# Performance work log

Hardware: AMD Instinct MI355X
Metric: run time of the kernel (lower is better)

Reference implementation:

```python
import jax, jax.numpy as jnp
import numpy as np
from jax import lax

B, T, I, H = 256, 512, 64, 512

def _uniform(key, shape, scale):
    return jax.random.uniform(key, shape, jnp.float32, -scale, scale)

def setup_inputs() -> dict:
    key = jax.random.key(0)
    ks = jax.random.split(key, 11)
    s = 1.0 / np.sqrt(H)
    return {
        "x": jax.random.normal(ks[0], (B, T, I), jnp.float32),
        "W_ih0": _uniform(ks[1], (4 * H, I), s),
        "W_hh0": _uniform(ks[2], (4 * H, H), s),
        "b_ih0": _uniform(ks[3], (4 * H,), s),
        "b_hh0": _uniform(ks[4], (4 * H,), s),
        "W_ih1": _uniform(ks[5], (4 * H, H), s),
        "W_hh1": _uniform(ks[6], (4 * H, H), s),
        "b_ih1": _uniform(ks[7], (4 * H,), s),
        "b_hh1": _uniform(ks[8], (4 * H,), s),
        "W_fc": _uniform(ks[9], (1, H), s),
        "b_fc": _uniform(ks[10], (1,), s),
    }

def _lstm_layer(x, W_ih, W_hh, b_ih, b_hh):
    # x: [B, T, in]; PyTorch gate order: i, f, g, o
    b, t, _ = x.shape
    h = W_hh.shape[1]
    # precompute input contribution for all timesteps: [B, T, 4H]
    xg = jnp.einsum('bti,gi->btg', x, W_ih) + b_ih + b_hh

    def step(carry, xg_t):
        h_prev, c_prev = carry
        gates = xg_t + h_prev @ W_hh.T  # [B, 4H]
        i_g, f_g, g_g, o_g = jnp.split(gates, 4, axis=-1)
        i_g = jax.nn.sigmoid(i_g)
        f_g = jax.nn.sigmoid(f_g)
        g_g = jnp.tanh(g_g)
        o_g = jax.nn.sigmoid(o_g)
        c = f_g * c_prev + i_g * g_g
        h_new = o_g * jnp.tanh(c)
        return (h_new, c), h_new

    init = (jnp.zeros((b, h), x.dtype), jnp.zeros((b, h), x.dtype))
    _, hs = lax.scan(step, init, xg.transpose(1, 0, 2))  # [T, B, H]
    return hs.transpose(1, 0, 2)  # [B, T, H]

def reference(x, W_ih0, W_hh0, b_ih0, b_hh0, W_ih1, W_hh1, b_ih1, b_hh1, W_fc, b_fc):
    out = _lstm_layer(x, W_ih0, W_hh0, b_ih0, b_hh0)
    # dropout p=0.0 between layers / before fc -> identity (eval semantics)
    out = _lstm_layer(out, W_ih1, W_hh1, b_ih1, b_hh1)
    hidden = out[:, -1, :]  # [B, H]
    return hidden @ W_fc.T + b_fc  # [B, 1]
```

## Files before the change

### kernel.cpp

```cpp
#include <hip/hip_runtime.h>

typedef __bf16 bf16x8 __attribute__((ext_vector_type(8)));
typedef float f32x4 __attribute__((ext_vector_type(4)));
typedef unsigned short u16;
typedef u16 ushort8 __attribute__((ext_vector_type(8)));

#define BB 256
#define TT 512
#define II 64
#define HH 512
#define SLOT 131072

#define OFF_H1RING 0x100000
#define OFF_H1FIN  0x180000
#define OFF_BAR    0x200000
#define OFF_XFRAG  0x210000
#define WS_NEED    (0x210000 + (size_t)(1 << 24))

__device__ __forceinline__ u16 f2bf(float f) {
  unsigned u = __builtin_bit_cast(unsigned, f);
  u = (u + 0x7FFFu + ((u >> 16) & 1u)) >> 16;
  return (u16)u;
}
__device__ __forceinline__ float sigmf(float v) {
  return 1.0f / (1.0f + __expf(-v));
}
__device__ __forceinline__ float tanh_s(float v) {
  float a = __builtin_fabsf(v);
  float e = __expf(-2.0f * a);
  float t = (1.0f - e) / (1.0f + e);
  return __builtin_copysignf(t, v);
}
__device__ __forceinline__ f32x4 mfma16(bf16x8 a, bf16x8 b, f32x4 c) {
  return __builtin_amdgcn_mfma_f32_16x16x32_bf16(a, b, c, 0, 0, 0);
}
__device__ __forceinline__ size_t fragoff(int R, int kk, int lane) {
  return ((size_t)(R * 16 + kk) * 64 + lane) * 8;
}
__device__ __forceinline__ bf16x8 ld_h8(const u16* p) {
  union { unsigned long long q[2]; ushort8 v; } u;
  u.q[0] = __hip_atomic_load((unsigned long long*)p, __ATOMIC_RELAXED,
                             __HIP_MEMORY_SCOPE_AGENT);
  u.q[1] = __hip_atomic_load((unsigned long long*)(p + 4), __ATOMIC_RELAXED,
                             __HIP_MEMORY_SCOPE_AGENT);
  return __builtin_bit_cast(bf16x8, u.v);
}
__device__ __forceinline__ bf16x8 ld_lds8(const u16* p) {
  return __builtin_bit_cast(bf16x8, *(const ushort8*)p);
}

__global__ void init_bar_k(unsigned* bar) {
  for (int i = threadIdx.x; i < 4096; i += blockDim.x) bar[i] = 0u;
}

__global__ void xpose_k(const float* __restrict__ x, u16* __restrict__ xfrag) {
  const size_t idx = (size_t)blockIdx.x * 256 + threadIdx.x;
  const int lane = idx & 63;
  const int kk = (idx >> 6) & 1;
  const int R = (idx >> 7) & 15;
  const int t = (int)(idx >> 11);
  const int row = R * 16 + (lane & 15);
  const int col = kk * 32 + (lane >> 4) * 8;
  const float* src = x + ((size_t)row * TT + t) * II + col;
  ushort8 v;
#pragma unroll
  for (int j = 0; j < 8; ++j) v[j] = f2bf(src[j]);
  *(ushort8*)(xfrag + idx * 8) = v;
}

__global__ __launch_bounds__(256, 1) void lstm_persist(
    const float* __restrict__ x, const u16* __restrict__ xfrag,
    const float* __restrict__ Wih0, const float* __restrict__ Whh0,
    const float* __restrict__ bih0, const float* __restrict__ bhh0,
    const float* __restrict__ Wih1, const float* __restrict__ Whh1,
    const float* __restrict__ bih1, const float* __restrict__ bhh1,
    u16* __restrict__ h0ring, u16* __restrict__ h1ring,
    float* __restrict__ h1fin, unsigned* __restrict__ barA,
    unsigned* __restrict__ barB) {
  __shared__ u16 w0s[32 * 600];
  __shared__ u16 w1s[32 * 1048];

  const int tid = threadIdx.x;
  const int lane = tid & 63;
  const int wid = tid >> 6;
  const int bid = blockIdx.x;
  const int ut = bid & 63, bt = bid >> 6;
  const int u0 = ut * 8;
  const int cc = lane & 15, grp = lane >> 4;

  unsigned* slotsA = barA + (size_t)bt * 256;
  unsigned* slotsB = barB + (size_t)bt * 256;

  {
    const int srow = tid >> 3, sub = tid & 7;
    const int g = (srow >> 3) * 512 + u0 + (srow & 7);
    const float* wih = Wih0 + (size_t)g * 64;
    const float* whh = Whh0 + (size_t)g * 512;
    const int e0 = sub * 72;
    for (int e = e0; e < e0 + 72; ++e) {
      float v = (e < 64) ? wih[e] : whh[e - 64];
      w0s[srow * 600 + e] = f2bf(v);
    }
  }
  {
    const int srow = tid >> 3, sub = tid & 7;
    const int g = (srow >> 3) * 512 + u0 + (srow & 7);
    const float* wih = Wih1 + (size_t)g * 512;
    const float* whh = Whh1 + (size_t)g * 512;
    const int e0 = sub * 128;
    for (int e = e0; e < e0 + 128; ++e) {
      float v = (e < 512) ? wih[e] : whh[e - 512];
      w1s[srow * 1048 + e] = f2bf(v);
    }
  }

  float bias0[2], bias1[2];
#pragma unroll
  for (int nf = 0; nf < 2; ++nf) {
    const int srow = nf * 16 + cc;
    const int g = (srow >> 3) * 512 + u0 + (srow & 7);
    bias0[nf] = bih0[g] + bhh0[g];
    bias1[nf] = bih1[g] + bhh1[g];
  }

  const int row0 = bt * 64 + wid * 16;
  const int Rw = bt * 4 + wid;
  const int arow = row0 + cc;
  const float* xbase = x + (size_t)arow * (TT * II) + grp * 8;
  const bool usexf = (xfrag != nullptr);
  float c0[4] = {0.f, 0.f, 0.f, 0.f};
  float c1[4] = {0.f, 0.f, 0.f, 0.f};

  ushort8 xpre[2];
  float xr[16];
  if (usexf) {
#pragma unroll
    for (int kk = 0; kk < 2; ++kk)
      xpre[kk] = *(const ushort8*)(xfrag + (size_t)Rw * 1024 +
                                   (size_t)kk * 512 + lane * 8);
  } else {
#pragma unroll
    for (int j = 0; j < 16; ++j) xr[j] = xbase[(j >> 3) * 32 + (j & 7)];
  }

  const int kkw = ut >> 2, lpb = (ut & 3) * 16;
  const int lb = grp * 8;

  __syncthreads();

#pragma unroll 1
  for (int s = 0; s <= 513; ++s) {
    const bool doL0 = (s < 512);
    bf16x8 hf[16];

    if (doL0) {
      f32x4 a00 = {bias0[0], bias0[0], bias0[0], bias0[0]};
      f32x4 a01 = {bias0[1], bias0[1], bias0[1], bias0[1]};
      bf16x8 xf[2];
      if (usexf) {
#pragma unroll
        for (int kk = 0; kk < 2; ++kk)
          xf[kk] = __builtin_bit_cast(bf16x8, xpre[kk]);
        const size_t sp = (size_t)((s + 1) & 511);
#pragma unroll
        for (int kk = 0; kk < 2; ++kk)
          xpre[kk] = *(const ushort8*)(xfrag + (sp * 16 + Rw) * 1024 +
                                       (size_t)kk * 512 + lane * 8);
      } else {
#pragma unroll
        for (int kk = 0; kk < 2; ++kk) {
          ushort8 t;
#pragma unroll
          for (int j = 0; j < 8; ++j) t[j] = f2bf(xr[kk * 8 + j]);
          xf[kk] = __builtin_bit_cast(bf16x8, t);
        }
        const size_t sp = (size_t)((s + 1) & 511);
#pragma unroll
        for (int j = 0; j < 16; ++j)
          xr[j] = xbase[sp * II + (j >> 3) * 32 + (j & 7)];
      }
      if (s >= 1) {
        const u16* p = h0ring + (size_t)((s - 1) & 3) * SLOT +
                       fragoff(Rw, 0, lane);
#pragma unroll
        for (int kk = 0; kk < 16; ++kk) hf[kk] = ld_h8(p + (size_t)kk * 512);
      }
#pragma unroll
      for (int kk = 0; kk < 2; ++kk) {
        bf16x8 bA = ld_lds8(&w0s[cc * 600 + kk * 32 + lb]);
        bf16x8 bB = ld_lds8(&w0s[(16 + cc) * 600 + kk * 32 + lb]);
        a00 = mfma16(xf[kk], bA, a00);
        a01 = mfma16(xf[kk], bB, a01);
      }
      if (s >= 1) {
#pragma unroll
        for (int kk = 0; kk < 16; ++kk) {
          bf16x8 bA = ld_lds8(&w0s[cc * 600 + (kk + 2) * 32 + lb]);
          bf16x8 bB = ld_lds8(&w0s[(16 + cc) * 600 + (kk + 2) * 32 + lb]);
          a00 = mfma16(hf[kk], bA, a00);
          a01 = mfma16(hf[kk], bB, a01);
        }
      }
      u16* h0wr = h0ring + (size_t)(s & 3) * SLOT;
#pragma unroll
      for (int r = 0; r < 4; ++r) {
        float f_p = __shfl_xor(a00[r], 8);
        float o_p = __shfl_xor(a01[r], 8);
        float ig = sigmf(a00[r]);
        float fg = sigmf(f_p);
        float gg = tanh_s(a01[r]);
        float og = sigmf(o_p);
        float cn = fg * c0[r] + ig * gg;
        c0[r] = cn;
        float hv = og * tanh_s(cn);
        unsigned myb = f2bf(hv);
        unsigned nb = (unsigned)__shfl_down((int)myb, 1);
        if (cc < 8 && (cc & 1) == 0) {
          unsigned* p = (unsigned*)(h0wr +
              fragoff(Rw, kkw, lpb + grp * 4 + r) + cc);
          __hip_atomic_store(p, myb | (nb << 16), __ATOMIC_RELAXED,
                             __HIP_MEMORY_SCOPE_AGENT);
        }
      }
      asm volatile("s_waitcnt vmcnt(0)" ::: "memory");
    }
    if (lane == 0)
      __hip_atomic_store(&slotsA[ut * 4 + wid], (unsigned)(s + 1),
                         __ATOMIC_RELAXED, __HIP_MEMORY_SCOPE_AGENT);

    if (s >= 2) {
      f32x4 a10 = {bias1[0], bias1[0], bias1[0], bias1[0]};
      f32x4 a11 = {bias1[1], bias1[1], bias1[1], bias1[1]};
      {
        const u16* p = h0ring + (size_t)((s - 2) & 3) * SLOT +
                       fragoff(Rw, 0, lane);
#pragma unroll
        for (int kk = 0; kk < 16; ++kk) hf[kk] = ld_h8(p + (size_t)kk * 512);
#pragma unroll
        for (int kk = 0; kk < 16; ++kk) {
          bf16x8 bA = ld_lds8(&w1s[cc * 1048 + kk * 32 + lb]);
          bf16x8 bB = ld_lds8(&w1s[(16 + cc) * 1048 + kk * 32 + lb]);
          a10 = mfma16(hf[kk], bA, a10);
          a11 = mfma16(hf[kk], bB, a11);
        }
      }
      if (s >= 3) {
        const unsigned tgtB = (unsigned)s;
        const unsigned long long* sl =
            (const unsigned long long*)slotsB + (size_t)lane * 2;
        for (;;) {
          unsigned long long q0 = __hip_atomic_load(sl, __ATOMIC_RELAXED,
                                                    __HIP_MEMORY_SCOPE_AGENT);
          unsigned long long q1 = __hip_atomic_load(sl + 1, __ATOMIC_RELAXED,
                                                    __HIP_MEMORY_SCOPE_AGENT);
          bool ok = ((unsigned)q0 >= tgtB) && ((unsigned)(q0 >> 32) >= tgtB) &&
                    ((unsigned)q1 >= tgtB) && ((unsigned)(q1 >> 32) >= tgtB);
          if (__all(ok)) break;
          __builtin_amdgcn_s_sleep(1);
        }
        const u16* p = h1ring + (size_t)((s - 3) & 1) * SLOT +
                       fragoff(Rw, 0, lane);
#pragma unroll
        for (int kk = 0; kk < 16; ++kk) hf[kk] = ld_h8(p + (size_t)kk * 512);
#pragma unroll
        for (int kk = 0; kk < 16; ++kk) {
          bf16x8 bA = ld_lds8(&w1s[cc * 1048 + (16 + kk) * 32 + lb]);
          bf16x8 bB = ld_lds8(&w1s[(16 + cc) * 1048 + (16 + kk) * 32 + lb]);
          a10 = mfma16(hf[kk], bA, a10);
          a11 = mfma16(hf[kk], bB, a11);
        }
      }
      u16* h1wr = h1ring + (size_t)((s - 2) & 1) * SLOT;
#pragma unroll
      for (int r = 0; r < 4; ++r) {
        float f_p = __shfl_xor(a10[r], 8);
        float o_p = __shfl_xor(a11[r], 8);
        float ig = sigmf(a10[r]);
        float fg = sigmf(f_p);
        float gg = tanh_s(a11[r]);
        float og = sigmf(o_p);
        float cn = fg * c1[r] + ig * gg;
        c1[r] = cn;
        float hv = og * tanh_s(cn);
        unsigned myb = f2bf(hv);
        unsigned nb = (unsigned)__shfl_down((int)myb, 1);
        if (cc < 8 && (cc & 1) == 0) {
          unsigned* p = (unsigned*)(h1wr +
              fragoff(Rw, kkw, lpb + grp * 4 + r) + cc);
          __hip_atomic_store(p, myb | (nb << 16), __ATOMIC_RELAXED,
                             __HIP_MEMORY_SCOPE_AGENT);
        }
        if (cc < 8 && s == 513)
          h1fin[(size_t)(row0 + grp * 4 + r) * HH + u0 + cc] = hv;
      }
      asm volatile("s_waitcnt vmcnt(0)" ::: "memory");
      if (lane == 0)
        __hip_atomic_store(&slotsB[ut * 4 + wid], (unsigned)(s + 1),
                           __ATOMIC_RELAXED, __HIP_MEMORY_SCOPE_AGENT);
    }

    if (s < 513) {
      __syncthreads();
      if (wid == 0) {
        const unsigned tgt = (unsigned)(s + 1);
        const unsigned long long* sl =
            (const unsigned long long*)slotsA + (size_t)lane * 2;
        for (;;) {
          unsigned long long q0 = __hip_atomic_load(sl, __ATOMIC_RELAXED,
                                                    __HIP_MEMORY_SCOPE_AGENT);
          unsigned long long q1 = __hip_atomic_load(sl + 1, __ATOMIC_RELAXED,
                                                    __HIP_MEMORY_SCOPE_AGENT);
          bool ok = ((unsigned)q0 >= tgt) && ((unsigned)(q0 >> 32) >= tgt) &&
                    ((unsigned)q1 >= tgt) && ((unsigned)(q1 >> 32) >= tgt);
          if (__all(ok)) break;
          __builtin_amdgcn_s_sleep(2);
        }
      }
      __syncthreads();
    }
  }
}

__global__ void fc_kernel(const float* __restrict__ h1fin,
                          const float* __restrict__ Wfc,
                          const float* __restrict__ bfc,
                          float* __restrict__ out) {
  const int wid = threadIdx.x >> 6, lane = threadIdx.x & 63;
  const int b = blockIdx.x * 4 + wid;
  float sum = 0.f;
#pragma unroll
  for (int j = 0; j < 8; ++j)
    sum += h1fin[(size_t)b * 512 + lane + 64 * j] * Wfc[lane + 64 * j];
#pragma unroll
  for (int m = 32; m; m >>= 1) sum += __shfl_xor(sum, m);
  if (lane == 0) out[b] = sum + bfc[0];
}

extern "C" void kernel_launch(void* const* d_in, const int* in_sizes, int n_in,
                              void* d_out, int out_size, void* d_ws, size_t ws_size,
                              hipStream_t stream) {
  const float* x    = (const float*)d_in[0];
  const float* Wih0 = (const float*)d_in[1];
  const float* Whh0 = (const float*)d_in[2];
  const float* bih0 = (const float*)d_in[3];
  const float* bhh0 = (const float*)d_in[4];
  const float* Wih1 = (const float*)d_in[5];
  const float* Whh1 = (const float*)d_in[6];
  const float* bih1 = (const float*)d_in[7];
  const float* bhh1 = (const float*)d_in[8];
  const float* Wfc  = (const float*)d_in[9];
  const float* bfc  = (const float*)d_in[10];

  char* ws = (char*)d_ws;
  u16* h0ring = (u16*)(ws);
  u16* h1ring = (u16*)(ws + OFF_H1RING);
  float* h1fin = (float*)(ws + OFF_H1FIN);
  unsigned* barA = (unsigned*)(ws + OFF_BAR);
  unsigned* barB = barA + 1024;
  u16* xfrag = (ws_size >= WS_NEED) ? (u16*)(ws + OFF_XFRAG) : nullptr;

  init_bar_k<<<1, 256, 0, stream>>>(barA);
  if (xfrag) xpose_k<<<4096, 256, 0, stream>>>(x, xfrag);
  lstm_persist<<<256, 256, 0, stream>>>(x, xfrag, Wih0, Whh0, bih0, bhh0,
                                        Wih1, Whh1, bih1, bhh1,
                                        h0ring, h1ring, h1fin, barA, barB);
  fc_kernel<<<64, 256, 0, stream>>>(h1fin, Wfc, bfc, (float*)d_out);
}
```

Measured before the change: 4.198 ms.

## Split LSTM layers onto separate persistent blocks with cross-layer flag sync

Before the change, each of the 256 persistent blocks computed both layer 0 and layer 1 for every step, with one wavefront-style barrier per step. Now 512 blocks are launched cooperatively: half run layer 0 and half run layer 1. They are coupled through per-step ready flags and 4-slot rings for h0 and h1, so the two layers pipeline across blocks and each block's per-step critical path shrinks. In exchange it needs 2 blocks per CU (launch bounds 2) and more polling on shared flags. Co-residency is only guaranteed when the cooperative launch succeeds; the fallback plain launch could deadlock.

```diff
diff --git a/kernel.cpp b/kernel.cpp
--- a/kernel.cpp
+++ b/kernel.cpp
@@ -12,10 +12,10 @@
 #define SLOT 131072
 
 #define OFF_H1RING 0x100000
-#define OFF_H1FIN  0x180000
-#define OFF_BAR    0x200000
-#define OFF_XFRAG  0x210000
-#define WS_NEED    (0x210000 + (size_t)(1 << 24))
+#define OFF_H1FIN  0x200000
+#define OFF_BAR    0x280000
+#define OFF_XFRAG  0x290000
+#define WS_NEED    (0x290000 + (size_t)(1 << 24))
 
 __device__ __forceinline__ u16 f2bf(float f) {
   unsigned u = __builtin_bit_cast(unsigned, f);
@@ -48,9 +48,24 @@
 __device__ __forceinline__ bf16x8 ld_lds8(const u16* p) {
   return __builtin_bit_cast(bf16x8, *(const ushort8*)p);
 }
+__device__ __forceinline__ void poll16(const unsigned* slots, unsigned tgt,
+                                       int lane) {
+  const unsigned long long* sl =
+      (const unsigned long long*)slots + (size_t)lane * 2;
+  for (;;) {
+    unsigned long long q0 = __hip_atomic_load(sl, __ATOMIC_RELAXED,
+                                              __HIP_MEMORY_SCOPE_AGENT);
+    unsigned long long q1 = __hip_atomic_load(sl + 1, __ATOMIC_RELAXED,
+                                              __HIP_MEMORY_SCOPE_AGENT);
+    bool ok = ((unsigned)q0 >= tgt) && ((unsigned)(q0 >> 32) >= tgt) &&
+              ((unsigned)q1 >= tgt) && ((unsigned)(q1 >> 32) >= tgt);
+    if (__all(ok)) break;
+    __builtin_amdgcn_s_sleep(2);
+  }
+}
 
 __global__ void init_bar_k(unsigned* bar) {
-  for (int i = threadIdx.x; i < 4096; i += blockDim.x) bar[i] = 0u;
+  for (int i = threadIdx.x; i < 2048; i += blockDim.x) bar[i] = 0u;
 }
 
 __global__ void xpose_k(const float* __restrict__ x, u16* __restrict__ xfrag) {
@@ -68,30 +83,34 @@
   *(ushort8*)(xfrag + idx * 8) = v;
 }
 
-__global__ __launch_bounds__(256, 1) void lstm_persist(
+__global__ __launch_bounds__(256, 2) void lstm_split(
     const float* __restrict__ x, const u16* __restrict__ xfrag,
     const float* __restrict__ Wih0, const float* __restrict__ Whh0,
     const float* __restrict__ bih0, const float* __restrict__ bhh0,
     const float* __restrict__ Wih1, const float* __restrict__ Whh1,
     const float* __restrict__ bih1, const float* __restrict__ bhh1,
     u16* __restrict__ h0ring, u16* __restrict__ h1ring,
-    float* __restrict__ h1fin, unsigned* __restrict__ barA,
-    unsigned* __restrict__ barB) {
-  __shared__ u16 w0s[32 * 600];
-  __shared__ u16 w1s[32 * 1048];
+    float* __restrict__ h1fin, unsigned* __restrict__ slotsA,
+    unsigned* __restrict__ slotsB) {
+  __shared__ u16 wsm[32 * 1048];
 
   const int tid = threadIdx.x;
   const int lane = tid & 63;
   const int wid = tid >> 6;
-  const int bid = blockIdx.x;
+  const bool isL1 = blockIdx.x >= 256;
+  const int bid = blockIdx.x & 255;
   const int ut = bid & 63, bt = bid >> 6;
   const int u0 = ut * 8;
   const int cc = lane & 15, grp = lane >> 4;
-
-  unsigned* slotsA = barA + (size_t)bt * 256;
-  unsigned* slotsB = barB + (size_t)bt * 256;
-
-  {
+  const int row0 = bt * 64 + wid * 16;
+  const int Rw = bt * 4 + wid;
+  const int kkw = ut >> 2, lpb = (ut & 3) * 16;
+  const int lb = grp * 8;
+
+  unsigned* myA = slotsA + (size_t)bt * 256;
+  unsigned* myB = slotsB + (size_t)bt * 256;
+
+  if (!isL1) {
     const int srow = tid >> 3, sub = tid & 7;
     const int g = (srow >> 3) * 512 + u0 + (srow & 7);
     const float* wih = Wih0 + (size_t)g * 64;
@@ -99,10 +118,9 @@
     const int e0 = sub * 72;
     for (int e = e0; e < e0 + 72; ++e) {
       float v = (e < 64) ? wih[e] : whh[e - 64];
-      w0s[srow * 600 + e] = f2bf(v);
-    }
-  }
-  {
+      wsm[srow * 600 + e] = f2bf(v);
+    }
+  } else {
     const int srow = tid >> 3, sub = tid & 7;
     const int g = (srow >> 3) * 512 + u0 + (srow & 7);
     const float* wih = Wih1 + (size_t)g * 512;
@@ -110,52 +128,55 @@
     const int e0 = sub * 128;
     for (int e = e0; e < e0 + 128; ++e) {
       float v = (e < 512) ? wih[e] : whh[e - 512];
-      w1s[srow * 1048 + e] = f2bf(v);
-    }
-  }
-
-  float bias0[2], bias1[2];
+      wsm[srow * 1048 + e] = f2bf(v);
+    }
+  }
+  __syncthreads();
+
+  float bias[2];
 #pragma unroll
   for (int nf = 0; nf < 2; ++nf) {
     const int srow = nf * 16 + cc;
     const int g = (srow >> 3) * 512 + u0 + (srow & 7);
-    bias0[nf] = bih0[g] + bhh0[g];
-    bias1[nf] = bih1[g] + bhh1[g];
-  }
-
-  const int row0 = bt * 64 + wid * 16;
-  const int Rw = bt * 4 + wid;
-  const int arow = row0 + cc;
-  const float* xbase = x + (size_t)arow * (TT * II) + grp * 8;
-  const bool usexf = (xfrag != nullptr);
-  float c0[4] = {0.f, 0.f, 0.f, 0.f};
-  float c1[4] = {0.f, 0.f, 0.f, 0.f};
-
-  ushort8 xpre[2];
-  float xr[16];
-  if (usexf) {
-#pragma unroll
-    for (int kk = 0; kk < 2; ++kk)
-      xpre[kk] = *(const ushort8*)(xfrag + (size_t)Rw * 1024 +
-                                   (size_t)kk * 512 + lane * 8);
-  } else {
-#pragma unroll
-    for (int j = 0; j < 16; ++j) xr[j] = xbase[(j >> 3) * 32 + (j & 7)];
-  }
-
-  const int kkw = ut >> 2, lpb = (ut & 3) * 16;
-  const int lb = grp * 8;
-
-  __syncthreads();
+    bias[nf] = isL1 ? (bih1[g] + bhh1[g]) : (bih0[g] + bhh0[g]);
+  }
+
+  float c[4] = {0.f, 0.f, 0.f, 0.f};
+  bf16x8 hf[16];
+
+  if (!isL1) {
+    const int arow = row0 + cc;
+    const float* xbase = x + (size_t)arow * (TT * II) + grp * 8;
+    const bool usexf = (xfrag != nullptr);
+    ushort8 xpre[2];
+    float xr[16];
+    if (usexf) {
+#pragma unroll
+      for (int kk = 0; kk < 2; ++kk)
+        xpre[kk] = *(const ushort8*)(xfrag + (size_t)Rw * 1024 +
+                                     (size_t)kk * 512 + lane * 8);
+    } else {
+#pragma unroll
+      for (int j = 0; j < 16; ++j) xr[j] = xbase[(j >> 3) * 32 + (j & 7)];
+    }
 
 #pragma unroll 1
-  for (int s = 0; s <= 513; ++s) {
-    const bool doL0 = (s < 512);
-    bf16x8 hf[16];
-
-    if (doL0) {
-      f32x4 a00 = {bias0[0], bias0[0], bias0[0], bias0[0]};
-      f32x4 a01 = {bias0[1], bias0[1], bias0[1], bias0[1]};
+    for (int s = 0; s < 512; ++s) {
+      if (wid == 0) {
+        if (s >= 1) poll16(myA, (unsigned)s, lane);
+        if (s >= 4) poll16(myB, (unsigned)(s - 3), lane);
+      }
+      __syncthreads();
+
+      if (s >= 1) {
+        const u16* p = h0ring + (size_t)((s - 1) & 3) * SLOT +
+                       fragoff(Rw, 0, lane);
+#pragma unroll
+        for (int kk = 0; kk < 16; ++kk) hf[kk] = ld_h8(p + (size_t)kk * 512);
+      }
+
+      f32x4 a0 = {bias[0], bias[0], bias[0], bias[0]};
+      f32x4 a1 = {bias[1], bias[1], bias[1], bias[1]};
       bf16x8 xf[2];
       if (usexf) {
 #pragma unroll
@@ -179,39 +200,33 @@
         for (int j = 0; j < 16; ++j)
           xr[j] = xbase[sp * II + (j >> 3) * 32 + (j & 7)];
       }
+#pragma unroll
+      for (int kk = 0; kk < 2; ++kk) {
+        bf16x8 bA = ld_lds8(&wsm[cc * 600 + kk * 32 + lb]);
+        bf16x8 bB = ld_lds8(&wsm[(16 + cc) * 600 + kk * 32 + lb]);
+        a0 = mfma16(xf[kk], bA, a0);
+        a1 = mfma16(xf[kk], bB, a1);
+      }
       if (s >= 1) {
-        const u16* p = h0ring + (size_t)((s - 1) & 3) * SLOT +
-                       fragoff(Rw, 0, lane);
-#pragma unroll
-        for (int kk = 0; kk < 16; ++kk) hf[kk] = ld_h8(p + (size_t)kk * 512);
-      }
-#pragma unroll
-      for (int kk = 0; kk < 2; ++kk) {
-        bf16x8 bA = ld_lds8(&w0s[cc * 600 + kk * 32 + lb]);
-        bf16x8 bB = ld_lds8(&w0s[(16 + cc) * 600 + kk * 32 + lb]);
-        a00 = mfma16(xf[kk], bA, a00);
-        a01 = mfma16(xf[kk], bB, a01);
-      }
-      if (s >= 1) {
 #pragma unroll
         for (int kk = 0; kk < 16; ++kk) {
-          bf16x8 bA = ld_lds8(&w0s[cc * 600 + (kk + 2) * 32 + lb]);
-          bf16x8 bB = ld_lds8(&w0s[(16 + cc) * 600 + (kk + 2) * 32 + lb]);
-          a00 = mfma16(hf[kk], bA, a00);
-          a01 = mfma16(hf[kk], bB, a01);
+          bf16x8 bA = ld_lds8(&wsm[cc * 600 + (kk + 2) * 32 + lb]);
+          bf16x8 bB = ld_lds8(&wsm[(16 + cc) * 600 + (kk + 2) * 32 + lb]);
+          a0 = mfma16(hf[kk], bA, a0);
+          a1 = mfma16(hf[kk], bB, a1);
         }
       }
       u16* h0wr = h0ring + (size_t)(s & 3) * SLOT;
 #pragma unroll
       for (int r = 0; r < 4; ++r) {
-        float f_p = __shfl_xor(a00[r], 8);
-        float o_p = __shfl_xor(a01[r], 8);
-        float ig = sigmf(a00[r]);
+        float f_p = __shfl_xor(a0[r], 8);
+        float o_p = __shfl_xor(a1[r], 8);
+        float ig = sigmf(a0[r]);
         float fg = sigmf(f_p);
-        float gg = tanh_s(a01[r]);
+        float gg = tanh_s(a1[r]);
         float og = sigmf(o_p);
-        float cn = fg * c0[r] + ig * gg;
-        c0[r] = cn;
+        float cn = fg * c[r] + ig * gg;
+        c[r] = cn;
         float hv = og * tanh_s(cn);
         unsigned myb = f2bf(hv);
         unsigned nb = (unsigned)__shfl_down((int)myb, 1);
@@ -223,64 +238,56 @@
         }
       }
       asm volatile("s_waitcnt vmcnt(0)" ::: "memory");
-    }
-    if (lane == 0)
-      __hip_atomic_store(&slotsA[ut * 4 + wid], (unsigned)(s + 1),
-                         __ATOMIC_RELAXED, __HIP_MEMORY_SCOPE_AGENT);
-
-    if (s >= 2) {
-      f32x4 a10 = {bias1[0], bias1[0], bias1[0], bias1[0]};
-      f32x4 a11 = {bias1[1], bias1[1], bias1[1], bias1[1]};
+      if (lane == 0)
+        __hip_atomic_store(&myA[ut * 4 + wid], (unsigned)(s + 1),
+                           __ATOMIC_RELAXED, __HIP_MEMORY_SCOPE_AGENT);
+    }
+  } else {
+#pragma unroll 1
+    for (int s = 0; s < 512; ++s) {
+      if (wid == 0) poll16(myA, (unsigned)(s + 1), lane);
+      __syncthreads();
+
       {
-        const u16* p = h0ring + (size_t)((s - 2) & 3) * SLOT +
+        const u16* p = h0ring + (size_t)(s & 3) * SLOT + fragoff(Rw, 0, lane);
+#pragma unroll
+        for (int kk = 0; kk < 16; ++kk) hf[kk] = ld_h8(p + (size_t)kk * 512);
+      }
+      f32x4 a0 = {bias[0], bias[0], bias[0], bias[0]};
+      f32x4 a1 = {bias[1], bias[1], bias[1], bias[1]};
+#pragma unroll
+      for (int kk = 0; kk < 16; ++kk) {
+        bf16x8 bA = ld_lds8(&wsm[cc * 1048 + kk * 32 + lb]);
+        bf16x8 bB = ld_lds8(&wsm[(16 + cc) * 1048 + kk * 32 + lb]);
+        a0 = mfma16(hf[kk], bA, a0);
+        a1 = mfma16(hf[kk], bB, a1);
+      }
+      if (wid == 0 && s >= 1) poll16(myB, (unsigned)s, lane);
+      __syncthreads();
+      if (s >= 1) {
+        const u16* p = h1ring + (size_t)((s - 1) & 3) * SLOT +
                        fragoff(Rw, 0, lane);
 #pragma unroll
         for (int kk = 0; kk < 16; ++kk) hf[kk] = ld_h8(p + (size_t)kk * 512);
 #pragma unroll
         for (int kk = 0; kk < 16; ++kk) {
-          bf16x8 bA = ld_lds8(&w1s[cc * 1048 + kk * 32 + lb]);
-          bf16x8 bB = ld_lds8(&w1s[(16 + cc) * 1048 + kk * 32 + lb]);
-          a10 = mfma16(hf[kk], bA, a10);
-          a11 = mfma16(hf[kk], bB, a11);
-        }
-      }
-      if (s >= 3) {
-        const unsigned tgtB = (unsigned)s;
-        const unsigned long long* sl =
-            (const unsigned long long*)slotsB + (size_t)lane * 2;
-        for (;;) {
-          unsigned long long q0 = __hip_atomic_load(sl, __ATOMIC_RELAXED,
-                                                    __HIP_MEMORY_SCOPE_AGENT);
-          unsigned long long q1 = __hip_atomic_load(sl + 1, __ATOMIC_RELAXED,
-                                                    __HIP_MEMORY_SCOPE_AGENT);
-          bool ok = ((unsigned)q0 >= tgtB) && ((unsigned)(q0 >> 32) >= tgtB) &&
-                    ((unsigned)q1 >= tgtB) && ((unsigned)(q1 >> 32) >= tgtB);
-          if (__all(ok)) break;
-          __builtin_amdgcn_s_sleep(1);
-        }
-        const u16* p = h1ring + (size_t)((s - 3) & 1) * SLOT +
-                       fragoff(Rw, 0, lane);
-#pragma unroll
-        for (int kk = 0; kk < 16; ++kk) hf[kk] = ld_h8(p + (size_t)kk * 512);
-#pragma unroll
-        for (int kk = 0; kk < 16; ++kk) {
-          bf16x8 bA = ld_lds8(&w1s[cc * 1048 + (16 + kk) * 32 + lb]);
-          bf16x8 bB = ld_lds8(&w1s[(16 + cc) * 1048 + (16 + kk) * 32 + lb]);
-          a10 = mfma16(hf[kk], bA, a10);
-          a11 = mfma16(hf[kk], bB, a11);
-        }
-      }
-      u16* h1wr = h1ring + (size_t)((s - 2) & 1) * SLOT;
+          bf16x8 bA = ld_lds8(&wsm[cc * 1048 + (16 + kk) * 32 + lb]);
+          bf16x8 bB = ld_lds8(&wsm[(16 + cc) * 1048 + (16 + kk) * 32 + lb]);
+          a0 = mfma16(hf[kk], bA, a0);
+          a1 = mfma16(hf[kk], bB, a1);
+        }
+      }
+      u16* h1wr = h1ring + (size_t)(s & 3) * SLOT;
 #pragma unroll
       for (int r = 0; r < 4; ++r) {
-        float f_p = __shfl_xor(a10[r], 8);
-        float o_p = __shfl_xor(a11[r], 8);
-        float ig = sigmf(a10[r]);
+        float f_p = __shfl_xor(a0[r], 8);
+        float o_p = __shfl_xor(a1[r], 8);
+        float ig = sigmf(a0[r]);
         float fg = sigmf(f_p);
-        float gg = tanh_s(a11[r]);
+        float gg = tanh_s(a1[r]);
         float og = sigmf(o_p);
-        float cn = fg * c1[r] + ig * gg;
-        c1[r] = cn;
+        float cn = fg * c[r] + ig * gg;
+        c[r] = cn;
         float hv = og * tanh_s(cn);
         unsigned myb = f2bf(hv);
         unsigned nb = (unsigned)__shfl_down((int)myb, 1);
@@ -290,33 +297,13 @@
           __hip_atomic_store(p, myb | (nb << 16), __ATOMIC_RELAXED,
                              __HIP_MEMORY_SCOPE_AGENT);
         }
-        if (cc < 8 && s == 513)
+        if (cc < 8 && s == 511)
           h1fin[(size_t)(row0 + grp * 4 + r) * HH + u0 + cc] = hv;
       }
       asm volatile("s_waitcnt vmcnt(0)" ::: "memory");
       if (lane == 0)
-        __hip_atomic_store(&slotsB[ut * 4 + wid], (unsigned)(s + 1),
+        __hip_atomic_store(&myB[ut * 4 + wid], (unsigned)(s + 1),
                            __ATOMIC_RELAXED, __HIP_MEMORY_SCOPE_AGENT);
-    }
-
-    if (s < 513) {
-      __syncthreads();
-      if (wid == 0) {
-        const unsigned tgt = (unsigned)(s + 1);
-        const unsigned long long* sl =
-            (const unsigned long long*)slotsA + (size_t)lane * 2;
-        for (;;) {
-          unsigned long long q0 = __hip_atomic_load(sl, __ATOMIC_RELAXED,
-                                                    __HIP_MEMORY_SCOPE_AGENT);
-          unsigned long long q1 = __hip_atomic_load(sl + 1, __ATOMIC_RELAXED,
-                                                    __HIP_MEMORY_SCOPE_AGENT);
-          bool ok = ((unsigned)q0 >= tgt) && ((unsigned)(q0 >> 32) >= tgt) &&
-                    ((unsigned)q1 >= tgt) && ((unsigned)(q1 >> 32) >= tgt);
-          if (__all(ok)) break;
-          __builtin_amdgcn_s_sleep(2);
-        }
-      }
-      __syncthreads();
     }
   }
 }
@@ -355,14 +342,25 @@
   u16* h0ring = (u16*)(ws);
   u16* h1ring = (u16*)(ws + OFF_H1RING);
   float* h1fin = (float*)(ws + OFF_H1FIN);
-  unsigned* barA = (unsigned*)(ws + OFF_BAR);
-  unsigned* barB = barA + 1024;
+  unsigned* slotsA = (unsigned*)(ws + OFF_BAR);
+  unsigned* slotsB = slotsA + 1024;
   u16* xfrag = (ws_size >= WS_NEED) ? (u16*)(ws + OFF_XFRAG) : nullptr;
 
-  init_bar_k<<<1, 256, 0, stream>>>(barA);
+  init_bar_k<<<1, 256, 0, stream>>>(slotsA);
   if (xfrag) xpose_k<<<4096, 256, 0, stream>>>(x, xfrag);
-  lstm_persist<<<256, 256, 0, stream>>>(x, xfrag, Wih0, Whh0, bih0, bhh0,
+
+  void* args[] = {(void*)&x, (void*)&xfrag,
+                  (void*)&Wih0, (void*)&Whh0, (void*)&bih0, (void*)&bhh0,
+                  (void*)&Wih1, (void*)&Whh1, (void*)&bih1, (void*)&bhh1,
+                  (void*)&h0ring, (void*)&h1ring, (void*)&h1fin,
+                  (void*)&slotsA, (void*)&slotsB};
+  hipError_t ce = hipLaunchCooperativeKernel((const void*)lstm_split,
+                                             dim3(512), dim3(256), args, 0,
+                                             stream);
+  if (ce != hipSuccess) {
+    lstm_split<<<512, 256, 0, stream>>>(x, xfrag, Wih0, Whh0, bih0, bhh0,
                                         Wih1, Whh1, bih1, bhh1,
-                                        h0ring, h1ring, h1fin, barA, barB);
+                                        h0ring, h1ring, h1fin, slotsA, slotsB);
+  }
   fc_kernel<<<64, 256, 0, stream>>>(h1fin, Wfc, bfc, (float*)d_out);
 }
```

Result: slower. 5.595 ms (+33.3%).

## Replace block-wide barrier with per-wave flag polling and shorten layer-1 skew

Applied to the files above, without the earlier changes.

Removes the __syncthreads plus wave-0 spin barrier at the end of each step. Each wave now polls only the 64 flags for its own row tile, laid out one slot per unit tile per wave. Layer 1 now runs one step behind layer 0 instead of two, reusing the h0 fragment already loaded for layer 0, which removes a second h0 load and one loop iteration. The cost is finer-grained polling by every wave and tighter cross-block dependencies, which could raise contention on the flag lines.

```diff
diff --git a/kernel.cpp b/kernel.cpp
--- a/kernel.cpp
+++ b/kernel.cpp
@@ -48,9 +48,19 @@
 __device__ __forceinline__ bf16x8 ld_lds8(const u16* p) {
   return __builtin_bit_cast(bf16x8, *(const ushort8*)p);
 }
+__device__ __forceinline__ void pollrow(const unsigned* row, unsigned tgt,
+                                        int lane) {
+  const unsigned* p = row + lane;
+  for (;;) {
+    unsigned v = __hip_atomic_load(p, __ATOMIC_RELAXED,
+                                   __HIP_MEMORY_SCOPE_AGENT);
+    if (__all(v >= tgt)) break;
+    __builtin_amdgcn_s_sleep(2);
+  }
+}
 
 __global__ void init_bar_k(unsigned* bar) {
-  for (int i = threadIdx.x; i < 4096; i += blockDim.x) bar[i] = 0u;
+  for (int i = threadIdx.x; i < 2048; i += blockDim.x) bar[i] = 0u;
 }
 
 __global__ void xpose_k(const float* __restrict__ x, u16* __restrict__ xfrag) {
@@ -75,8 +85,8 @@
     const float* __restrict__ Wih1, const float* __restrict__ Whh1,
     const float* __restrict__ bih1, const float* __restrict__ bhh1,
     u16* __restrict__ h0ring, u16* __restrict__ h1ring,
-    float* __restrict__ h1fin, unsigned* __restrict__ barA,
-    unsigned* __restrict__ barB) {
+    float* __restrict__ h1fin, unsigned* __restrict__ slotsA,
+    unsigned* __restrict__ slotsB) {
   __shared__ u16 w0s[32 * 600];
   __shared__ u16 w1s[32 * 1048];
 
@@ -88,8 +98,8 @@
   const int u0 = ut * 8;
   const int cc = lane & 15, grp = lane >> 4;
 
-  unsigned* slotsA = barA + (size_t)bt * 256;
-  unsigned* slotsB = barB + (size_t)bt * 256;
+  unsigned* rowA = slotsA + (size_t)bt * 256 + wid * 64;
+  unsigned* rowB = slotsB + (size_t)bt * 256 + wid * 64;
 
   {
     const int srow = tid >> 3, sub = tid & 7;
@@ -148,10 +158,19 @@
 
   __syncthreads();
 
+  bf16x8 hcur[16];
+
 #pragma unroll 1
-  for (int s = 0; s <= 513; ++s) {
+  for (int s = 0; s <= 512; ++s) {
     const bool doL0 = (s < 512);
-    bf16x8 hf[16];
+
+    if (s >= 1) {
+      pollrow(rowA, (unsigned)s, lane);
+      const u16* p = h0ring + (size_t)((s - 1) & 3) * SLOT +
+                     fragoff(Rw, 0, lane);
+#pragma unroll
+      for (int kk = 0; kk < 16; ++kk) hcur[kk] = ld_h8(p + (size_t)kk * 512);
+    }
 
     if (doL0) {
       f32x4 a00 = {bias0[0], bias0[0], bias0[0], bias0[0]};
@@ -179,12 +198,6 @@
         for (int j = 0; j < 16; ++j)
           xr[j] = xbase[sp * II + (j >> 3) * 32 + (j & 7)];
       }
-      if (s >= 1) {
-        const u16* p = h0ring + (size_t)((s - 1) & 3) * SLOT +
-                       fragoff(Rw, 0, lane);
-#pragma unroll
-        for (int kk = 0; kk < 16; ++kk) hf[kk] = ld_h8(p + (size_t)kk * 512);
-      }
 #pragma unroll
       for (int kk = 0; kk < 2; ++kk) {
         bf16x8 bA = ld_lds8(&w0s[cc * 600 + kk * 32 + lb]);
@@ -197,8 +210,8 @@
         for (int kk = 0; kk < 16; ++kk) {
           bf16x8 bA = ld_lds8(&w0s[cc * 600 + (kk + 2) * 32 + lb]);
           bf16x8 bB = ld_lds8(&w0s[(16 + cc) * 600 + (kk + 2) * 32 + lb]);
-          a00 = mfma16(hf[kk], bA, a00);
-          a01 = mfma16(hf[kk], bB, a01);
+          a00 = mfma16(hcur[kk], bA, a00);
+          a01 = mfma16(hcur[kk], bB, a01);
         }
       }
       u16* h0wr = h0ring + (size_t)(s & 3) * SLOT;
@@ -223,54 +236,39 @@
         }
       }
       asm volatile("s_waitcnt vmcnt(0)" ::: "memory");
-    }
-    if (lane == 0)
-      __hip_atomic_store(&slotsA[ut * 4 + wid], (unsigned)(s + 1),
-                         __ATOMIC_RELAXED, __HIP_MEMORY_SCOPE_AGENT);
-
-    if (s >= 2) {
+      if (lane == 0)
+        __hip_atomic_store(&rowA[ut], (unsigned)(s + 1), __ATOMIC_RELAXED,
+                           __HIP_MEMORY_SCOPE_AGENT);
+    }
+
+    if (s >= 1) {
+      bf16x8 h1f[16];
+      if (s >= 2) {
+        pollrow(rowB, (unsigned)s, lane);
+        const u16* p = h1ring + (size_t)((s - 2) & 1) * SLOT +
+                       fragoff(Rw, 0, lane);
+#pragma unroll
+        for (int kk = 0; kk < 16; ++kk) h1f[kk] = ld_h8(p + (size_t)kk * 512);
+      }
       f32x4 a10 = {bias1[0], bias1[0], bias1[0], bias1[0]};
       f32x4 a11 = {bias1[1], bias1[1], bias1[1], bias1[1]};
-      {
-        const u16* p = h0ring + (size_t)((s - 2) & 3) * SLOT +
-                       fragoff(Rw, 0, lane);
-#pragma unroll
-        for (int kk = 0; kk < 16; ++kk) hf[kk] = ld_h8(p + (size_t)kk * 512);
-#pragma unroll
-        for (int kk = 0; kk < 16; ++kk) {
-          bf16x8 bA = ld_lds8(&w1s[cc * 1048 + kk * 32 + lb]);
-          bf16x8 bB = ld_lds8(&w1s[(16 + cc) * 1048 + kk * 32 + lb]);
-          a10 = mfma16(hf[kk], bA, a10);
-          a11 = mfma16(hf[kk], bB, a11);
-        }
-      }
-      if (s >= 3) {
-        const unsigned tgtB = (unsigned)s;
-        const unsigned long long* sl =
-            (const unsigned long long*)slotsB + (size_t)lane * 2;
-        for (;;) {
-          unsigned long long q0 = __hip_atomic_load(sl, __ATOMIC_RELAXED,
-                                                    __HIP_MEMORY_SCOPE_AGENT);
-          unsigned long long q1 = __hip_atomic_load(sl + 1, __ATOMIC_RELAXED,
-                                                    __HIP_MEMORY_SCOPE_AGENT);
-          bool ok = ((unsigned)q0 >= tgtB) && ((unsigned)(q0 >> 32) >= tgtB) &&
-                    ((unsigned)q1 >= tgtB) && ((unsigned)(q1 >> 32) >= tgtB);
-          if (__all(ok)) break;
-          __builtin_amdgcn_s_sleep(1);
-        }
-        const u16* p = h1ring + (size_t)((s - 3) & 1) * SLOT +
-                       fragoff(Rw, 0, lane);
-#pragma unroll
-        for (int kk = 0; kk < 16; ++kk) hf[kk] = ld_h8(p + (size_t)kk * 512);
+#pragma unroll
+      for (int kk = 0; kk < 16; ++kk) {
+        bf16x8 bA = ld_lds8(&w1s[cc * 1048 + kk * 32 + lb]);
+        bf16x8 bB = ld_lds8(&w1s[(16 + cc) * 1048 + kk * 32 + lb]);
+        a10 = mfma16(hcur[kk], bA, a10);
+        a11 = mfma16(hcur[kk], bB, a11);
+      }
+      if (s >= 2) {
 #pragma unroll
         for (int kk = 0; kk < 16; ++kk) {
           bf16x8 bA = ld_lds8(&w1s[cc * 1048 + (16 + kk) * 32 + lb]);
           bf16x8 bB = ld_lds8(&w1s[(16 + cc) * 1048 + (16 + kk) * 32 + lb]);
-          a10 = mfma16(hf[kk], bA, a10);
-          a11 = mfma16(hf[kk], bB, a11);
-        }
-      }
-      u16* h1wr = h1ring + (size_t)((s - 2) & 1) * SLOT;
+          a10 = mfma16(h1f[kk], bA, a10);
+          a11 = mfma16(h1f[kk], bB, a11);
+        }
+      }
+      u16* h1wr = h1ring + (size_t)((s - 1) & 1) * SLOT;
 #pragma unroll
       for (int r = 0; r < 4; ++r) {
         float f_p = __shfl_xor(a10[r], 8);
@@ -290,33 +288,13 @@
           __hip_atomic_store(p, myb | (nb << 16), __ATOMIC_RELAXED,
                              __HIP_MEMORY_SCOPE_AGENT);
         }
-        if (cc < 8 && s == 513)
+        if (cc < 8 && s == 512)
           h1fin[(size_t)(row0 + grp * 4 + r) * HH + u0 + cc] = hv;
       }
       asm volatile("s_waitcnt vmcnt(0)" ::: "memory");
       if (lane == 0)
-        __hip_atomic_store(&slotsB[ut * 4 + wid], (unsigned)(s + 1),
-                           __ATOMIC_RELAXED, __HIP_MEMORY_SCOPE_AGENT);
-    }
-
-    if (s < 513) {
-      __syncthreads();
-      if (wid == 0) {
-        const unsigned tgt = (unsigned)(s + 1);
-        const unsigned long long* sl =
-            (const unsigned long long*)slotsA + (size_t)lane * 2;
-        for (;;) {
-          unsigned long long q0 = __hip_atomic_load(sl, __ATOMIC_RELAXED,
-                                                    __HIP_MEMORY_SCOPE_AGENT);
-          unsigned long long q1 = __hip_atomic_load(sl + 1, __ATOMIC_RELAXED,
-                                                    __HIP_MEMORY_SCOPE_AGENT);
-          bool ok = ((unsigned)q0 >= tgt) && ((unsigned)(q0 >> 32) >= tgt) &&
-                    ((unsigned)q1 >= tgt) && ((unsigned)(q1 >> 32) >= tgt);
-          if (__all(ok)) break;
-          __builtin_amdgcn_s_sleep(2);
-        }
-      }
-      __syncthreads();
+        __hip_atomic_store(&rowB[ut], (unsigned)(s + 1), __ATOMIC_RELAXED,
+                           __HIP_MEMORY_SCOPE_AGENT);
     }
   }
 }
@@ -355,14 +333,14 @@
   u16* h0ring = (u16*)(ws);
   u16* h1ring = (u16*)(ws + OFF_H1RING);
   float* h1fin = (float*)(ws + OFF_H1FIN);
-  unsigned* barA = (unsigned*)(ws + OFF_BAR);
-  unsigned* barB = barA + 1024;
+  unsigned* slotsA = (unsigned*)(ws + OFF_BAR);
+  unsigned* slotsB = slotsA + 1024;
   u16* xfrag = (ws_size >= WS_NEED) ? (u16*)(ws + OFF_XFRAG) : nullptr;
 
-  init_bar_k<<<1, 256, 0, stream>>>(barA);
+  init_bar_k<<<1, 256, 0, stream>>>(slotsA);
   if (xfrag) xpose_k<<<4096, 256, 0, stream>>>(x, xfrag);
   lstm_persist<<<256, 256, 0, stream>>>(x, xfrag, Wih0, Whh0, bih0, bhh0,
                                         Wih1, Whh1, bih1, bhh1,
-                                        h0ring, h1ring, h1fin, barA, barB);
+                                        h0ring, h1ring, h1fin, slotsA, slotsB);
   fc_kernel<<<64, 256, 0, stream>>>(h1fin, Wfc, bfc, (float*)d_out);
 }
```

Measured after the change: 3.772 ms. -10.1%, faster.
